# Optimization experiments

Measured on AMD Instinct MI355X. Metric: run time of the kernel, lower is better.

Reference implementation:

```python
import jax, jax.numpy as jnp
import numpy as np

B, S, N, H, D = 8, 2048, 8, 1024, 64  # batch, seq, n_tasks, hidden, dense_size
T = 50.0  # temperature (fusion_config['temperature']=True)


def setup_inputs() -> dict:
    key = jax.random.key(0)
    ks = jax.random.split(key, 10)
    return {
        "query": jax.random.normal(ks[0], (B, S, H), dtype=jnp.float32),
        "key": jax.random.normal(ks[1], (B, S, N, D), dtype=jnp.float32),
        "value": jax.random.normal(ks[2], (B, S, N, H), dtype=jnp.float32),
        "attention_mask": jax.random.randint(ks[3], (B, S), 0, 2, dtype=jnp.int32),
        # nn.Linear weights are [out, in]
        "Wq": jax.random.normal(ks[4], (D, H), dtype=jnp.float32) * 0.02,
        "bq": jnp.zeros((D,), dtype=jnp.float32),
        "Wk": jax.random.normal(ks[5], (D, D), dtype=jnp.float32) * 0.02,
        "bk": jnp.zeros((D,), dtype=jnp.float32),
        "Wv": jax.random.normal(ks[6], (H, H), dtype=jnp.float32) * 0.02,
        "bv": jnp.zeros((H,), dtype=jnp.float32),
    }


def reference(query, key, value, attention_mask, Wq, bq, Wk, bk, Wv, bv):
    # mask==0 means valid token (per original: (attention_mask == 0).float())
    mask = (attention_mask == 0).astype(jnp.float32)          # [B, S]
    length = jnp.sum(mask, axis=1)                            # [B]
    # masked mean pooling (instead of repeat-based broadcasting)
    key_sent = jnp.einsum("bs,bsnd->bnd", mask, key) / length[:, None, None]   # [B, N, D]
    query_sent = jnp.einsum("bs,bsh->bh", mask, query) / length[:, None]       # [B, H]
    query_enc = query_sent @ Wq.T + bq                        # [B, D]
    key_enc = key_sent @ Wk.T + bk                            # [B, N, D]
    value_enc = jnp.einsum("bsnh,oh->bsno", value, Wv) + bv   # [B, S, N, H]
    scores = jnp.einsum("bnd,bd->bn", key_enc, query_enc)     # [B, N]
    probs = jax.nn.softmax(scores / T, axis=-1)               # [B, N]
    result = jnp.einsum("bn,bsnh->bsh", probs, value_enc)     # [B, S, H]
    return result
```

## Files before the change

kernel.cpp:

```cpp
#include <hip/hip_runtime.h>
#include <hip/hip_bf16.h>
#include <stdint.h>

#define BB 8
#define SS 2048
#define NTASK 8
#define HH 1024
#define DD 64
#define TEMP 50.0f

typedef __attribute__((ext_vector_type(8))) short short8;
typedef __attribute__((ext_vector_type(4))) float floatx4;

static __device__ __forceinline__ unsigned short f2bf(float f) {
  union { float f; unsigned int u; } v; v.f = f;
  unsigned int u = v.u;
  unsigned int r = u + 0x7FFFu + ((u >> 16) & 1u);
  return (unsigned short)(r >> 16);
}

#define SCHUNKS 64
#define SCHUNK (SS / SCHUNKS)

__global__ void pool_kernel(const float* __restrict__ query,
                            const float* __restrict__ key,
                            const int* __restrict__ amask,
                            float* __restrict__ qsum,
                            float* __restrict__ ksum,
                            float* __restrict__ lensum)
{
  __shared__ float valid[SCHUNK];
  int b = blockIdx.x >> 6;
  int chunk = blockIdx.x & 63;
  int s0 = chunk * SCHUNK;
  int tid = threadIdx.x;
  if (tid < SCHUNK) valid[tid] = (amask[b * SS + s0 + tid] == 0) ? 1.0f : 0.0f;
  __syncthreads();

  {
    const float* qb = query + ((size_t)b * SS + s0) * HH;
    int h0 = tid * 4;
    floatx4 acc = {0.f, 0.f, 0.f, 0.f};
    for (int s = 0; s < SCHUNK; ++s) {
      floatx4 v = *(const floatx4*)(qb + (size_t)s * HH + h0);
      acc += valid[s] * v;
    }
    atomicAdd(&qsum[b * HH + h0 + 0], acc.x);
    atomicAdd(&qsum[b * HH + h0 + 1], acc.y);
    atomicAdd(&qsum[b * HH + h0 + 2], acc.z);
    atomicAdd(&qsum[b * HH + h0 + 3], acc.w);
  }
  if (tid < 128) {
    const float* kb = key + ((size_t)b * SS + s0) * (NTASK * DD);
    int i0 = tid * 4;
    floatx4 acc = {0.f, 0.f, 0.f, 0.f};
    for (int s = 0; s < SCHUNK; ++s) {
      floatx4 v = *(const floatx4*)(kb + (size_t)s * (NTASK * DD) + i0);
      acc += valid[s] * v;
    }
    atomicAdd(&ksum[b * NTASK * DD + i0 + 0], acc.x);
    atomicAdd(&ksum[b * NTASK * DD + i0 + 1], acc.y);
    atomicAdd(&ksum[b * NTASK * DD + i0 + 2], acc.z);
    atomicAdd(&ksum[b * NTASK * DD + i0 + 3], acc.w);
  }
  if (tid == 0) {
    float c = 0.f;
    for (int s = 0; s < SCHUNK; ++s) c += valid[s];
    atomicAdd(&lensum[b], c);
  }
}

__global__ void qenc_kernel(const float* __restrict__ qsum,
                            const float* __restrict__ lensum,
                            const float* __restrict__ Wq,
                            const float* __restrict__ bq,
                            float* __restrict__ qe)
{
  int b = blockIdx.x >> 6;
  int d = blockIdx.x & 63;
  int tid = threadIdx.x;
  const float* wr = Wq + (size_t)d * HH;
  const float* qs = qsum + (size_t)b * HH;
  float acc = 0.f;
  for (int h = tid; h < HH; h += 256) acc += qs[h] * wr[h];
  __shared__ float red[256];
  red[tid] = acc;
  __syncthreads();
  for (int off = 128; off > 0; off >>= 1) {
    if (tid < off) red[tid] += red[tid + off];
    __syncthreads();
  }
  if (tid == 0) qe[blockIdx.x] = red[0] / lensum[b] + bq[d];
}

__global__ void probs_kernel(const float* __restrict__ ksum,
                             const float* __restrict__ lensum,
                             const float* __restrict__ qe_g,
                             const float* __restrict__ Wk,
                             const float* __restrict__ bk,
                             float* __restrict__ probs)
{
  __shared__ float ke[BB * NTASK * DD];
  __shared__ float qe[BB * DD];
  __shared__ float sc[BB * NTASK];
  int tid = threadIdx.x;
  for (int i = tid; i < BB * DD; i += 256) qe[i] = qe_g[i];
  for (int idx = tid; idx < BB * NTASK * DD; idx += 256) {
    int d = idx & 63;
    int bn = idx >> 6;
    int b = bn >> 3;
    const float* wr = Wk + d * DD;
    const float* ks = ksum + bn * DD;
    float acc = 0.f;
#pragma unroll 8
    for (int d2 = 0; d2 < DD; ++d2) acc += ks[d2] * wr[d2];
    ke[idx] = acc / lensum[b] + bk[d];
  }
  __syncthreads();
  if (tid < BB * NTASK) {
    int b = tid >> 3;
    float acc = 0.f;
    for (int d = 0; d < DD; ++d) acc += ke[tid * DD + d] * qe[b * DD + d];
    sc[tid] = acc / TEMP;
  }
  __syncthreads();
  if (tid < BB * NTASK) {
    int b = tid >> 3;
    float mx = -1e30f;
    for (int n = 0; n < NTASK; ++n) mx = fmaxf(mx, sc[b * NTASK + n]);
    float den = 0.f;
    for (int n = 0; n < NTASK; ++n) den += expf(sc[b * NTASK + n] - mx);
    probs[tid] = expf(sc[tid] - mx) / den;
  }
}

__global__ void vmix_kernel(const float* __restrict__ value,
                            const float* __restrict__ probs,
                            unsigned short* __restrict__ vmix)
{
  __shared__ float p[NTASK];
  int bs = blockIdx.x;
  int b = bs >> 11;
  if (threadIdx.x < NTASK) p[threadIdx.x] = probs[b * NTASK + threadIdx.x];
  __syncthreads();
  const float* vp = value + (size_t)bs * NTASK * HH;
  int h0 = threadIdx.x * 4;
  floatx4 acc = {0.f, 0.f, 0.f, 0.f};
#pragma unroll
  for (int n = 0; n < NTASK; ++n) {
    floatx4 v = *(const floatx4*)(vp + (size_t)n * HH + h0);
    acc += p[n] * v;
  }
  union { unsigned short us[4]; uint2 u2; } pk;
  pk.us[0] = f2bf(acc.x);
  pk.us[1] = f2bf(acc.y);
  pk.us[2] = f2bf(acc.z);
  pk.us[3] = f2bf(acc.w);
  *(uint2*)(vmix + (size_t)bs * HH + h0) = pk.u2;
}

__global__ void wvsplit_kernel(const float* __restrict__ Wv,
                               unsigned short* __restrict__ WvB)
{
  int i = (blockIdx.x * 256 + threadIdx.x) * 4;
  floatx4 v = *(const floatx4*)(Wv + i);
  union { unsigned short us[4]; uint2 u2; } pk;
  pk.us[0] = f2bf(v.x);
  pk.us[1] = f2bf(v.y);
  pk.us[2] = f2bf(v.z);
  pk.us[3] = f2bf(v.w);
  *(uint2*)(WvB + i) = pk.u2;
}

#define BM 128
#define BN 128
#define BK 32

#define GLDS16(gsrc, ldst)                                                     \
  __builtin_amdgcn_global_load_lds(                                            \
      (const __attribute__((address_space(1))) void*)(gsrc),                   \
      (__attribute__((address_space(3))) void*)(ldst), 16, 0, 0)

__global__ __launch_bounds__(256)
void gemm_kernel(const unsigned short* __restrict__ A,
                 const unsigned short* __restrict__ Bm,
                 const float* __restrict__ bv,
                 float* __restrict__ C)
{
  const int N = HH;
  const int K = HH;
  __shared__ unsigned short As[BM * BK];
  __shared__ unsigned short Bs[BN * BK];

  int tid = threadIdx.x;
  int m0 = (int)blockIdx.x * BM;
  int n0 = (int)blockIdx.y * BN;
  int wave = tid >> 6;
  int lane = tid & 63;
  int wr = wave >> 1, wc = wave & 1;
  int quad = lane >> 4;
  int l16 = lane & 15;

  floatx4 acc[4][4] = {};

  int srow = wave * 32 + (lane >> 2);
  int schk = (lane & 3) * 8;
  const unsigned short* ga0 = A  + (size_t)(m0 + srow) * K + schk;
  const unsigned short* ga1 = ga0 + (size_t)16 * K;
  const unsigned short* gb0 = Bm + (size_t)(n0 + srow) * K + schk;
  const unsigned short* gb1 = gb0 + (size_t)16 * K;
  unsigned short* la0 = As + (wave * 32) * BK;
  unsigned short* la1 = As + (wave * 32 + 16) * BK;
  unsigned short* lb0 = Bs + (wave * 32) * BK;
  unsigned short* lb1 = Bs + (wave * 32 + 16) * BK;

  const int NKB = K / BK;
  for (int kb = 0; kb < NKB; ++kb) {
    int ko = kb * BK;
    GLDS16(ga0 + ko, la0);
    GLDS16(ga1 + ko, la1);
    GLDS16(gb0 + ko, lb0);
    GLDS16(gb1 + ko, lb1);
    __syncthreads();

    short8 af[4], bf[4];
#pragma unroll
    for (int mi = 0; mi < 4; ++mi)
      af[mi] = *(const short8*)&As[(wr * 64 + mi * 16 + l16) * BK + quad * 8];
#pragma unroll
    for (int ni = 0; ni < 4; ++ni)
      bf[ni] = *(const short8*)&Bs[(wc * 64 + ni * 16 + l16) * BK + quad * 8];
#pragma unroll
    for (int mi = 0; mi < 4; ++mi)
#pragma unroll
      for (int ni = 0; ni < 4; ++ni)
        acc[mi][ni] = __builtin_amdgcn_mfma_f32_16x16x32_bf16(
            af[mi], bf[ni], acc[mi][ni], 0, 0, 0);
    __syncthreads();
  }

#pragma unroll
  for (int ni = 0; ni < 4; ++ni) {
    int gn = n0 + wc * 64 + ni * 16 + l16;
    float bvv = bv[gn];
#pragma unroll
    for (int mi = 0; mi < 4; ++mi) {
      int gm = m0 + wr * 64 + mi * 16 + quad * 4;
#pragma unroll
      for (int r = 0; r < 4; ++r)
        C[(size_t)(gm + r) * N + gn] = acc[mi][ni][r] + bvv;
    }
  }
}

extern "C" void kernel_launch(void* const* d_in, const int* in_sizes, int n_in,
                              void* d_out, int out_size, void* d_ws, size_t ws_size,
                              hipStream_t stream) {
  const float* query = (const float*)d_in[0];
  const float* key   = (const float*)d_in[1];
  const float* value = (const float*)d_in[2];
  const int*   amask = (const int*)d_in[3];
  const float* Wq = (const float*)d_in[4];
  const float* bq = (const float*)d_in[5];
  const float* Wk = (const float*)d_in[6];
  const float* bk = (const float*)d_in[7];
  const float* Wv = (const float*)d_in[8];
  const float* bv = (const float*)d_in[9];
  float* out = (float*)d_out;

  char* ws = (char*)d_ws;
  unsigned short* vmix = (unsigned short*)(ws);
  unsigned short* WvB  = (unsigned short*)(ws + (size_t)33554432);
  float* qsum   = (float*)(ws + (size_t)35651584);
  float* ksum   = qsum + BB * HH;
  float* lensum = ksum + BB * NTASK * DD;
  float* probs  = lensum + BB;
  float* qe     = probs + BB * NTASK;

  hipMemsetAsync(qsum, 0, (size_t)(BB * HH + BB * NTASK * DD + BB) * sizeof(float), stream);

  pool_kernel<<<BB * SCHUNKS, 256, 0, stream>>>(query, key, amask, qsum, ksum, lensum);
  qenc_kernel<<<BB * DD, 256, 0, stream>>>(qsum, lensum, Wq, bq, qe);
  probs_kernel<<<1, 256, 0, stream>>>(ksum, lensum, qe, Wk, bk, probs);
  vmix_kernel<<<BB * SS, 256, 0, stream>>>(value, probs, vmix);
  wvsplit_kernel<<<(HH * HH) / (256 * 4), 256, 0, stream>>>(Wv, WvB);
  dim3 grid(BB * SS / BM, HH / BN);
  gemm_kernel<<<grid, 256, 0, stream>>>(vmix, WvB, bv, out);
}
```

Baseline: 873.3 us.

## Fuse Wv conversion into pooling, skip masked rows, batch vmix rows, swizzle GEMM grid

Moves the fp32-to-bf16 conversion of Wv into the pooling kernel, which removes one kernel launch. Masked-out sequence rows are now skipped in pooling, so their loads are never issued. vmix processes 8 rows per block with nontemporal loads. The GEMM uses a flat grid remapped so neighbouring tiles land on the same XCD, and it writes its output with nontemporal stores. Together these aim to cut launch overhead and memory traffic and to improve L2 locality, at the cost of divergent branches in pooling and less parallelism in vmix.

```diff
diff --git a/kernel.cpp b/kernel.cpp
--- a/kernel.cpp
+++ b/kernel.cpp
@@ -25,9 +25,11 @@
 __global__ void pool_kernel(const float* __restrict__ query,
                             const float* __restrict__ key,
                             const int* __restrict__ amask,
+                            const float* __restrict__ Wv,
                             float* __restrict__ qsum,
                             float* __restrict__ ksum,
-                            float* __restrict__ lensum)
+                            float* __restrict__ lensum,
+                            unsigned short* __restrict__ WvB)
 {
   __shared__ float valid[SCHUNK];
   int b = blockIdx.x >> 6;
@@ -38,12 +40,26 @@
   __syncthreads();
 
   {
+    size_t i = ((size_t)blockIdx.x * 256 + tid) * 8;
+    floatx4 v0 = *(const floatx4*)(Wv + i);
+    floatx4 v1 = *(const floatx4*)(Wv + i + 4);
+    union { unsigned short us[8]; uint4 u4; } pk;
+    pk.us[0] = f2bf(v0.x); pk.us[1] = f2bf(v0.y);
+    pk.us[2] = f2bf(v0.z); pk.us[3] = f2bf(v0.w);
+    pk.us[4] = f2bf(v1.x); pk.us[5] = f2bf(v1.y);
+    pk.us[6] = f2bf(v1.z); pk.us[7] = f2bf(v1.w);
+    *(uint4*)(WvB + i) = pk.u4;
+  }
+
+  {
     const float* qb = query + ((size_t)b * SS + s0) * HH;
     int h0 = tid * 4;
     floatx4 acc = {0.f, 0.f, 0.f, 0.f};
     for (int s = 0; s < SCHUNK; ++s) {
-      floatx4 v = *(const floatx4*)(qb + (size_t)s * HH + h0);
-      acc += valid[s] * v;
+      if (valid[s] != 0.0f) {
+        floatx4 v = *(const floatx4*)(qb + (size_t)s * HH + h0);
+        acc += v;
+      }
     }
     atomicAdd(&qsum[b * HH + h0 + 0], acc.x);
     atomicAdd(&qsum[b * HH + h0 + 1], acc.y);
@@ -55,8 +71,10 @@
     int i0 = tid * 4;
     floatx4 acc = {0.f, 0.f, 0.f, 0.f};
     for (int s = 0; s < SCHUNK; ++s) {
-      floatx4 v = *(const floatx4*)(kb + (size_t)s * (NTASK * DD) + i0);
-      acc += valid[s] * v;
+      if (valid[s] != 0.0f) {
+        floatx4 v = *(const floatx4*)(kb + (size_t)s * (NTASK * DD) + i0);
+        acc += v;
+      }
     }
     atomicAdd(&ksum[b * NTASK * DD + i0 + 0], acc.x);
     atomicAdd(&ksum[b * NTASK * DD + i0 + 1], acc.y);
@@ -134,42 +152,33 @@
   }
 }
 
+#define VROWS 8
 __global__ void vmix_kernel(const float* __restrict__ value,
                             const float* __restrict__ probs,
                             unsigned short* __restrict__ vmix)
 {
   __shared__ float p[NTASK];
-  int bs = blockIdx.x;
-  int b = bs >> 11;
+  int bs0 = blockIdx.x * VROWS;
+  int b = bs0 >> 11;
   if (threadIdx.x < NTASK) p[threadIdx.x] = probs[b * NTASK + threadIdx.x];
   __syncthreads();
-  const float* vp = value + (size_t)bs * NTASK * HH;
   int h0 = threadIdx.x * 4;
-  floatx4 acc = {0.f, 0.f, 0.f, 0.f};
-#pragma unroll
-  for (int n = 0; n < NTASK; ++n) {
-    floatx4 v = *(const floatx4*)(vp + (size_t)n * HH + h0);
-    acc += p[n] * v;
-  }
-  union { unsigned short us[4]; uint2 u2; } pk;
-  pk.us[0] = f2bf(acc.x);
-  pk.us[1] = f2bf(acc.y);
-  pk.us[2] = f2bf(acc.z);
-  pk.us[3] = f2bf(acc.w);
-  *(uint2*)(vmix + (size_t)bs * HH + h0) = pk.u2;
-}
-
-__global__ void wvsplit_kernel(const float* __restrict__ Wv,
-                               unsigned short* __restrict__ WvB)
-{
-  int i = (blockIdx.x * 256 + threadIdx.x) * 4;
-  floatx4 v = *(const floatx4*)(Wv + i);
-  union { unsigned short us[4]; uint2 u2; } pk;
-  pk.us[0] = f2bf(v.x);
-  pk.us[1] = f2bf(v.y);
-  pk.us[2] = f2bf(v.z);
-  pk.us[3] = f2bf(v.w);
-  *(uint2*)(WvB + i) = pk.u2;
+  for (int r = 0; r < VROWS; ++r) {
+    const float* vp = value + (size_t)(bs0 + r) * NTASK * HH;
+    floatx4 acc = {0.f, 0.f, 0.f, 0.f};
+#pragma unroll
+    for (int n = 0; n < NTASK; ++n) {
+      floatx4 v = __builtin_nontemporal_load(
+          (const floatx4*)(vp + (size_t)n * HH + h0));
+      acc += p[n] * v;
+    }
+    union { unsigned short us[4]; uint2 u2; } pk;
+    pk.us[0] = f2bf(acc.x);
+    pk.us[1] = f2bf(acc.y);
+    pk.us[2] = f2bf(acc.z);
+    pk.us[3] = f2bf(acc.w);
+    *(uint2*)(vmix + (size_t)(bs0 + r) * HH + h0) = pk.u2;
+  }
 }
 
 #define BM 128
@@ -177,7 +186,7 @@
 #define BK 32
 
 #define GLDS16(gsrc, ldst)                                                     \
-  __builtin_amdgcn_global_load_lds(                                            \
+  __builtin_amdgcn_global_load_lds(                                           \
       (const __attribute__((address_space(1))) void*)(gsrc),                   \
       (__attribute__((address_space(3))) void*)(ldst), 16, 0, 0)
 
@@ -193,8 +202,13 @@
   __shared__ unsigned short Bs[BN * BK];
 
   int tid = threadIdx.x;
-  int m0 = (int)blockIdx.x * BM;
-  int n0 = (int)blockIdx.y * BN;
+  int bflat = (int)blockIdx.x;
+  int xcd = bflat & 7;
+  int j = bflat >> 3;
+  int ytile = j & 7;
+  int xtile = xcd + ((j >> 3) << 3);
+  int m0 = xtile * BM;
+  int n0 = ytile * BN;
   int wave = tid >> 6;
   int lane = tid & 63;
   int wr = wave >> 1, wc = wave & 1;
@@ -248,7 +262,8 @@
       int gm = m0 + wr * 64 + mi * 16 + quad * 4;
 #pragma unroll
       for (int r = 0; r < 4; ++r)
-        C[(size_t)(gm + r) * N + gn] = acc[mi][ni][r] + bvv;
+        __builtin_nontemporal_store(acc[mi][ni][r] + bvv,
+                                    &C[(size_t)(gm + r) * N + gn]);
     }
   }
 }
@@ -279,11 +294,9 @@
 
   hipMemsetAsync(qsum, 0, (size_t)(BB * HH + BB * NTASK * DD + BB) * sizeof(float), stream);
 
-  pool_kernel<<<BB * SCHUNKS, 256, 0, stream>>>(query, key, amask, qsum, ksum, lensum);
+  pool_kernel<<<BB * SCHUNKS, 256, 0, stream>>>(query, key, amask, Wv, qsum, ksum, lensum, WvB);
   qenc_kernel<<<BB * DD, 256, 0, stream>>>(qsum, lensum, Wq, bq, qe);
   probs_kernel<<<1, 256, 0, stream>>>(ksum, lensum, qe, Wk, bk, probs);
-  vmix_kernel<<<BB * SS, 256, 0, stream>>>(value, probs, vmix);
-  wvsplit_kernel<<<(HH * HH) / (256 * 4), 256, 0, stream>>>(Wv, WvB);
-  dim3 grid(BB * SS / BM, HH / BN);
-  gemm_kernel<<<grid, 256, 0, stream>>>(vmix, WvB, bv, out);
-}
+  vmix_kernel<<<BB * SS / VROWS, 256, 0, stream>>>(value, probs, vmix);
+  gemm_kernel<<<1024, 256, 0, stream>>>(vmix, WvB, bv, out);
+}
```

After: 857.0 us. Within noise of the previous version (-1.9%).
